# Kernel optimization log

Measured on AMD Instinct MI355X. Metric: run time of the kernel, lower is better.

The kernel has to match this reference:

```python
import jax, jax.numpy as jnp
import numpy as np

B, S_BERT, L_WORD, D = 64, 512, 256, 768
REDUC, HID, TAGS, POL = 400, 100, 5, 4


def _make_positions():
    # Each word spans 1-2 consecutive subwords; 256 words * max 2 <= 512 subwords.
    rng = np.random.default_rng(0)
    lens = rng.integers(1, 3, size=(B, L_WORD))          # [B, L] in {1,2}
    starts = np.cumsum(lens, axis=1) - lens              # exclusive prefix sum
    ends = starts + lens - 1                             # inclusive end, <= 511
    return jnp.asarray(np.stack([starts, ends], axis=-1), dtype=jnp.int32)


def setup_inputs() -> dict:
    key = jax.random.key(0)
    ks = jax.random.split(key, 8)
    s = 0.02
    return {
        "bert_vectors": jax.random.normal(ks[0], (B, S_BERT, D), jnp.float32),
        "positions": _make_positions(),
        "W_reduc": jax.random.normal(ks[1], (D, REDUC), jnp.float32) * s,
        "b_reduc": jnp.zeros((REDUC,), jnp.float32),
        "W_ap": jax.random.normal(ks[2], (REDUC, HID), jnp.float32) * s,
        "b_ap": jnp.zeros((HID,), jnp.float32),
        "W_op": jax.random.normal(ks[3], (REDUC, HID), jnp.float32) * s,
        "b_op": jnp.zeros((HID,), jnp.float32),
        "W_ap_tag": jax.random.normal(ks[4], (HID, TAGS), jnp.float32) * s,
        "b_ap_tag": jnp.zeros((TAGS,), jnp.float32),
        "W_op_tag": jax.random.normal(ks[5], (HID, TAGS), jnp.float32) * s,
        "b_op_tag": jnp.zeros((TAGS,), jnp.float32),
        # Biaffine: bias=(True, False) -> in1 gets a ones column: [HID+1, POL*HID]
        "W_bi": jax.random.normal(ks[6], (HID + 1, POL * HID), jnp.float32) * s,
    }


def _segment_mean(vectors, positions):
    # vectors: [B, S, D]; positions: [B, L, 2] inclusive (start, end) spans.
    cs = jnp.cumsum(vectors, axis=1)
    cs = jnp.concatenate([jnp.zeros_like(cs[:, :1]), cs], axis=1)   # [B, S+1, D]
    starts = positions[..., 0]
    ends = positions[..., 1]
    hi = jnp.take_along_axis(cs, (ends + 1)[..., None], axis=1)     # [B, L, D]
    lo = jnp.take_along_axis(cs, starts[..., None], axis=1)
    lens = (ends - starts + 1).astype(vectors.dtype)[..., None]
    return (hi - lo) / lens                                          # [B, L, D]


def reference(bert_vectors, positions, W_reduc, b_reduc, W_ap, b_ap, W_op, b_op,
              W_ap_tag, b_ap_tag, W_op_tag, b_op_tag, W_bi):
    pooled = _segment_mean(bert_vectors, positions)                  # [B, L, D]
    h = jax.nn.relu(pooled @ W_reduc + b_reduc)                      # [B, L, 400]
    ap = jax.nn.relu(h @ W_ap + b_ap)                                # [B, L, 100]
    op = jax.nn.relu(h @ W_op + b_op)                                # [B, L, 100]
    ap_out = ap @ W_ap_tag + b_ap_tag                                # [B, L, T]
    op_out = op @ W_op_tag + b_op_tag                                # [B, L, T]
    # Biaffine with bias=(True, False)
    ones = jnp.ones_like(ap[..., :1])
    a1 = jnp.concatenate([ap, ones], axis=-1)                        # [B, L, 101]
    affine = (a1 @ W_bi).reshape(ap.shape[0], ap.shape[1], POL, HID) # [B, L1, P, H]
    triplet = jnp.einsum('biph,bjh->bjip', affine, op)               # [B, L2, L1, P]
    return ap_out, op_out, triplet
```

## Files before the change

kernel.cpp:

```cpp
#include <hip/hip_runtime.h>
#include <hip/hip_bf16.h>

#define B_    64
#define S_    512
#define L_    256
#define D_    768
#define RED_  400
#define REDP_ 512
#define KEFF_ 416
#define HID_  100
#define HIDP_ 128
#define TAGS_ 5
#define POL_  4
#define NBI_  512
#define NAO_  256
#define BL_   (B_ * L_)

typedef __attribute__((ext_vector_type(8))) short short8;
typedef __attribute__((ext_vector_type(4))) float f32x4;
typedef __attribute__((ext_vector_type(4))) unsigned short u16x4;

#define GLOAD_LDS16(gp, lp) __builtin_amdgcn_global_load_lds( \
    (const __attribute__((address_space(1))) void*)(gp),      \
    (__attribute__((address_space(3))) void*)(lp), 16, 0, 0)

__device__ inline float bf2f(unsigned short u) {
    union { unsigned int i; float f; } c; c.i = ((unsigned)u) << 16; return c.f;
}
__device__ inline unsigned short f2bf(float f) {
    __hip_bfloat16 h = __float2bfloat16(f);
    unsigned short u;
    __builtin_memcpy(&u, &h, 2);
    return u;
}

#define SZ0 393216
#define SZ1 131072
#define SZ2 65536
#define SZ3 512
#define SZ4 256
#define PREP_TOT (SZ0 + SZ1 + SZ2 + SZ3 + SZ4)
#define PREP_BLOCKS ((PREP_TOT + 255) / 256)

__global__ __launch_bounds__(256) void prep_kernel(
    const float* __restrict__ W_reduc, const float* __restrict__ b_reduc,
    const float* __restrict__ W_ap, const float* __restrict__ b_ap,
    const float* __restrict__ W_op, const float* __restrict__ b_op,
    const float* __restrict__ W_bi,
    unsigned short* __restrict__ WtR, unsigned short* __restrict__ WtAO,
    unsigned short* __restrict__ WtBi,
    float* __restrict__ bR, float* __restrict__ bAO, float* __restrict__ bBi)
{
    int idx = blockIdx.x * 256 + threadIdx.x;
    if (idx < SZ0) {
        int n = idx / D_, k = idx - n * D_;
        float v = (n < RED_) ? W_reduc[(size_t)k * RED_ + n] : 0.f;
        WtR[idx] = f2bf(v);
    } else if (idx < SZ0 + SZ1) {
        int i = idx - SZ0;
        int n = i >> 9, k = i & 511;
        float v = 0.f;
        if (k < RED_) {
            if (n < HID_)                      v = W_ap[(size_t)k * HID_ + n];
            else if (n >= 128 && n < 128+HID_) v = W_op[(size_t)k * HID_ + (n-128)];
        }
        WtAO[i] = f2bf(v);
    } else if (idx < SZ0 + SZ1 + SZ2) {
        int i = idx - SZ0 - SZ1;
        int n = i >> 7, k = i & 127;
        int p = n >> 7, h = n & 127;
        float v = (h < HID_ && k < HID_) ? W_bi[(size_t)k * RED_ + p * HID_ + h] : 0.f;
        WtBi[i] = f2bf(v);
        if (k == 0) bBi[n] = (h < HID_) ? W_bi[(size_t)HID_ * RED_ + p * HID_ + h] : 0.f;
    } else if (idx < SZ0 + SZ1 + SZ2 + SZ3) {
        int n = idx - SZ0 - SZ1 - SZ2;
        bR[n] = (n < RED_) ? b_reduc[n] : 0.f;
    } else if (idx < PREP_TOT) {
        int n = idx - SZ0 - SZ1 - SZ2 - SZ3;
        bAO[n] = (n < 128) ? ((n < HID_) ? b_ap[n] : 0.f)
                           : (((n-128) < HID_) ? b_op[n-128] : 0.f);
    }
}

__global__ __launch_bounds__(256) void gemm1_seg_kernel(
    const float* __restrict__ bert, const int* __restrict__ pos,
    const short* __restrict__ Bt, const float* __restrict__ bias,
    unsigned short* __restrict__ Co)
{
    __shared__ __align__(16) short lds[2][10240];

    const int t  = threadIdx.x;
    const int wv = t >> 6;
    const int ln = t & 63;
    const int bm  = blockIdx.x * 64;
    const int bnh = blockIdx.y * 256;
    const int batch = bm >> 8;

    const int srow = t >> 2;
    const int skc  = (t & 3) * 8;

    const int r = bm + srow;
    const int s = pos[r * 2 + 0];
    const int e = pos[r * 2 + 1];
    const size_t rb0 = ((size_t)batch * S_ + s) * D_;
    const size_t rb1 = ((size_t)batch * S_ + e) * D_;

    f32x4 acc[4][4] = {};
    const int NT = D_ >> 5;

    {
        #pragma unroll
        for (int q = 0; q < 4; ++q) {
            const short* g = Bt + (size_t)(bnh + q * 64 + srow) * D_ + skc;
            GLOAD_LDS16(g, &lds[0][2048 + q * 2048 + wv * 512]);
        }
        f32x4 x0 = *(const f32x4*)(bert + rb0 + skc);
        f32x4 x1 = *(const f32x4*)(bert + rb0 + skc + 4);
        f32x4 y0 = *(const f32x4*)(bert + rb1 + skc);
        f32x4 y1 = *(const f32x4*)(bert + rb1 + skc + 4);
        f32x4 s0 = (x0 + y0) * 0.5f;
        f32x4 s1 = (x1 + y1) * 0.5f;
        union { short8 v; unsigned short u[8]; } o;
        #pragma unroll
        for (int j = 0; j < 4; ++j) { o.u[j] = f2bf(s0[j]); o.u[4+j] = f2bf(s1[j]); }
        *(short8*)(&lds[0][srow * 32 + skc]) = o.v;
    }
    __syncthreads();

    int cur = 0;
    const int lr = ln & 15;
    const int lk = (ln >> 4) * 8;

    for (int kt = 0; kt < NT; ++kt) {
        const bool more = (kt + 1 < NT);
        f32x4 x0, x1, y0, y1;
        if (more) {
            int col = (kt + 1) * 32 + skc;
            x0 = *(const f32x4*)(bert + rb0 + col);
            x1 = *(const f32x4*)(bert + rb0 + col + 4);
            y0 = *(const f32x4*)(bert + rb1 + col);
            y1 = *(const f32x4*)(bert + rb1 + col + 4);
            #pragma unroll
            for (int q = 0; q < 4; ++q) {
                const short* g = Bt + (size_t)(bnh + q * 64 + srow) * D_ + (kt + 1) * 32 + skc;
                GLOAD_LDS16(g, &lds[cur ^ 1][2048 + q * 2048 + wv * 512]);
            }
        }

        const short* As = &lds[cur][0];
        const short* Bs = &lds[cur][2048];
        short8 a[4], b[4];
        #pragma unroll
        for (int fi = 0; fi < 4; ++fi)
            a[fi] = *(const short8*)(As + (fi * 16 + lr) * 32 + lk);
        #pragma unroll
        for (int fj = 0; fj < 4; ++fj)
            b[fj] = *(const short8*)(Bs + (wv * 64 + fj * 16 + lr) * 32 + lk);
        #pragma unroll
        for (int fi = 0; fi < 4; ++fi)
            #pragma unroll
            for (int fj = 0; fj < 4; ++fj)
                acc[fi][fj] = __builtin_amdgcn_mfma_f32_16x16x32_bf16(
                    a[fi], b[fj], acc[fi][fj], 0, 0, 0);

        if (more) {
            f32x4 s0 = (x0 + y0) * 0.5f;
            f32x4 s1 = (x1 + y1) * 0.5f;
            union { short8 v; unsigned short u[8]; } o;
            #pragma unroll
            for (int j = 0; j < 4; ++j) { o.u[j] = f2bf(s0[j]); o.u[4+j] = f2bf(s1[j]); }
            *(short8*)(&lds[cur ^ 1][srow * 32 + skc]) = o.v;
        }

        __syncthreads();
        cur ^= 1;
    }

    const int row0 = bm + (ln >> 4) * 4;
    const int col0 = bnh + wv * 64 + lr;
    #pragma unroll
    for (int fi = 0; fi < 4; ++fi)
        #pragma unroll
        for (int rr = 0; rr < 4; ++rr) {
            int row = row0 + fi * 16 + rr;
            #pragma unroll
            for (int fj = 0; fj < 4; ++fj) {
                int col = col0 + fj * 16;
                float v = fmaxf(acc[fi][fj][rr] + bias[col], 0.f);
                Co[(size_t)row * REDP_ + col] = f2bf(v);
            }
        }
}

__global__ __launch_bounds__(256) void gemm23_tag_kernel(
    const short* __restrict__ A, const short* __restrict__ Bt,
    const float* __restrict__ bias,
    unsigned short* __restrict__ apOut, unsigned short* __restrict__ opOut,
    const float* __restrict__ Wap_tag, const float* __restrict__ bap_tag,
    const float* __restrict__ Wop_tag, const float* __restrict__ bop_tag,
    float* __restrict__ out_tag)
{
    __shared__ __align__(16) short lds[2][8192];
    __shared__ float tagf[128 * 101];
    __shared__ float Wtag[HID_ * TAGS_];
    __shared__ float Btag[TAGS_];

    const int t  = threadIdx.x;
    const int wv = t >> 6;
    const int ln = t & 63;
    const int wm = wv >> 1;
    const int wn = wv & 1;
    const int bm = blockIdx.x * 128;
    const int bn = blockIdx.y * 128;
    const int half = blockIdx.y;

    const float* Wt = half ? Wop_tag : Wap_tag;
    const float* bt = half ? bop_tag : bap_tag;
    for (int i = t; i < HID_ * TAGS_; i += 256) Wtag[i] = Wt[i];
    if (t < TAGS_) Btag[t] = bt[t];

    const int srow = t >> 2;
    const int skc  = (t & 3) * 8;
    const int NT = KEFF_ >> 5;

    f32x4 acc[4][4] = {};

    {
        #pragma unroll
        for (int q = 0; q < 2; ++q) {
            const short* g = A + (size_t)(bm + q * 64 + srow) * REDP_ + skc;
            GLOAD_LDS16(g, &lds[0][q * 2048 + wv * 512]);
        }
        #pragma unroll
        for (int q = 0; q < 2; ++q) {
            const short* g = Bt + (size_t)(bn + q * 64 + srow) * REDP_ + skc;
            GLOAD_LDS16(g, &lds[0][4096 + q * 2048 + wv * 512]);
        }
    }
    __syncthreads();

    int cur = 0;
    const int lr = ln & 15;
    const int lk = (ln >> 4) * 8;

    for (int kt = 0; kt < NT; ++kt) {
        if (kt + 1 < NT) {
            int k0 = (kt + 1) << 5;
            #pragma unroll
            for (int q = 0; q < 2; ++q) {
                const short* g = A + (size_t)(bm + q * 64 + srow) * REDP_ + k0 + skc;
                GLOAD_LDS16(g, &lds[cur ^ 1][q * 2048 + wv * 512]);
            }
            #pragma unroll
            for (int q = 0; q < 2; ++q) {
                const short* g = Bt + (size_t)(bn + q * 64 + srow) * REDP_ + k0 + skc;
                GLOAD_LDS16(g, &lds[cur ^ 1][4096 + q * 2048 + wv * 512]);
            }
        }

        const short* As = &lds[cur][0];
        const short* Bs = &lds[cur][4096];
        short8 a[4], b[4];
        #pragma unroll
        for (int fi = 0; fi < 4; ++fi)
            a[fi] = *(const short8*)(As + (wm * 64 + fi * 16 + lr) * 32 + lk);
        #pragma unroll
        for (int fj = 0; fj < 4; ++fj)
            b[fj] = *(const short8*)(Bs + (wn * 64 + fj * 16 + lr) * 32 + lk);
        #pragma unroll
        for (int fi = 0; fi < 4; ++fi)
            #pragma unroll
            for (int fj = 0; fj < 4; ++fj)
                acc[fi][fj] = __builtin_amdgcn_mfma_f32_16x16x32_bf16(
                    a[fi], b[fj], acc[fi][fj], 0, 0, 0);

        __syncthreads();
        cur ^= 1;
    }

    unsigned short* Co = half ? opOut : apOut;
    const int rl0 = wm * 64 + (ln >> 4) * 4;
    const int cl0 = wn * 64 + lr;
    #pragma unroll
    for (int fi = 0; fi < 4; ++fi)
        #pragma unroll
        for (int r = 0; r < 4; ++r) {
            int rl = rl0 + fi * 16 + r;
            #pragma unroll
            for (int fj = 0; fj < 4; ++fj) {
                int cl = cl0 + fj * 16;
                float v = fmaxf(acc[fi][fj][r] + bias[bn + cl], 0.f);
                Co[(size_t)(bm + rl) * 128 + cl] = f2bf(v);
                if (cl < 101) tagf[rl * 101 + cl] = v;
            }
        }
    __syncthreads();

    if (t < 128) {
        float s[TAGS_];
        #pragma unroll
        for (int g = 0; g < TAGS_; ++g) s[g] = Btag[g];
        const float* rowp = &tagf[t * 101];
        for (int k = 0; k < HID_; ++k) {
            float x = rowp[k];
            #pragma unroll
            for (int g = 0; g < TAGS_; ++g) s[g] += x * Wtag[k * TAGS_ + g];
        }
        float* o = out_tag + (size_t)half * (BL_ * TAGS_) + (size_t)(bm + t) * TAGS_;
        #pragma unroll
        for (int g = 0; g < TAGS_; ++g) o[g] = s[g];
    }
}

__global__ __launch_bounds__(256) void affine_kernel(
    const short* __restrict__ ap, const short* __restrict__ WtBi,
    const float* __restrict__ bBi, unsigned short* __restrict__ affine)
{
    __shared__ __align__(16) short As[16384];
    __shared__ __align__(16) short Bs[16384];

    const int t  = threadIdx.x;
    const int wv = t >> 6;
    const int ln = t & 63;
    const int wm = wv >> 1;
    const int wn = wv & 1;
    const int bm = blockIdx.x * 128;
    const int bn = blockIdx.y * 128;

    const int rsub = ln >> 2;
    const int j8   = (ln & 3) * 8;

    #pragma unroll
    for (int i = 0; i < 8; ++i) {
        int ks = i >> 1, hf = i & 1;
        int rloc = wv * 32 + hf * 16;
        const short* gA = ap + (size_t)(bm + rloc + rsub) * HIDP_ + ks * 32 + j8;
        GLOAD_LDS16(gA, &As[ks * 4096 + rloc * 32]);
        const short* gB = WtBi + (size_t)(bn + rloc + rsub) * HIDP_ + ks * 32 + j8;
        GLOAD_LDS16(gB, &Bs[ks * 4096 + rloc * 32]);
    }
    __syncthreads();

    const int lr = ln & 15;
    const int lk = (ln >> 4) * 8;
    f32x4 acc[4][4] = {};

    #pragma unroll
    for (int ks = 0; ks < 4; ++ks) {
        short8 a[4], b[4];
        #pragma unroll
        for (int fi = 0; fi < 4; ++fi)
            a[fi] = *(const short8*)(As + ks * 4096 + (wm * 64 + fi * 16 + lr) * 32 + lk);
        #pragma unroll
        for (int fj = 0; fj < 4; ++fj)
            b[fj] = *(const short8*)(Bs + ks * 4096 + (wn * 64 + fj * 16 + lr) * 32 + lk);
        #pragma unroll
        for (int fi = 0; fi < 4; ++fi)
            #pragma unroll
            for (int fj = 0; fj < 4; ++fj)
                acc[fi][fj] = __builtin_amdgcn_mfma_f32_16x16x32_bf16(
                    a[fi], b[fj], acc[fi][fj], 0, 0, 0);
    }

    const int row0 = bm + wm * 64 + (ln >> 4) * 4;
    const int col0 = bn + wn * 64 + lr;
    #pragma unroll
    for (int fi = 0; fi < 4; ++fi)
        #pragma unroll
        for (int r = 0; r < 4; ++r) {
            int row = row0 + fi * 16 + r;
            #pragma unroll
            for (int fj = 0; fj < 4; ++fj) {
                int col = col0 + fj * 16;
                affine[(size_t)row * NBI_ + col] = f2bf(acc[fi][fj][r] + bBi[col]);
            }
        }
}

__global__ __launch_bounds__(256) void triplet_kernel(
    const short* __restrict__ op, const short* __restrict__ affine,
    float* __restrict__ out)
{
    __shared__ __align__(16) short As[16384];
    __shared__ __align__(16) short Bs[16384];

    const int t  = threadIdx.x;
    const int wv = t >> 6;
    const int ln = t & 63;
    const int wm = wv >> 1;
    const int wn = wv & 1;
    const int bm = blockIdx.x * 128;
    const int bn = blockIdx.y * 128;
    const int b  = blockIdx.z;

    const short* Ab = op     + (size_t)b * 256 * HIDP_;
    const short* Bb = affine + (size_t)b * 256 * NBI_;

    const int rsub = ln >> 2;
    const int j8   = (ln & 3) * 8;

    #pragma unroll
    for (int i = 0; i < 8; ++i) {
        int ks = i >> 1, hf = i & 1;
        int rloc = wv * 32 + hf * 16;
        const short* gA = Ab + (size_t)(bm + rloc + rsub) * HIDP_ + ks * 32 + j8;
        GLOAD_LDS16(gA, &As[ks * 4096 + rloc * 32]);
        int ip = bn + rloc + rsub;
        const short* gB = Bb + (size_t)(ip >> 2) * NBI_ + (ip & 3) * HIDP_ + ks * 32 + j8;
        GLOAD_LDS16(gB, &Bs[ks * 4096 + rloc * 32]);
    }
    __syncthreads();

    const int lr = ln & 15;
    const int lk = (ln >> 4) * 8;
    f32x4 acc[4][4] = {};

    #pragma unroll
    for (int ks = 0; ks < 4; ++ks) {
        short8 a[4], bf[4];
        #pragma unroll
        for (int fi = 0; fi < 4; ++fi)
            a[fi] = *(const short8*)(As + ks * 4096 + (wm * 64 + fi * 16 + lr) * 32 + lk);
        #pragma unroll
        for (int fj = 0; fj < 4; ++fj)
            bf[fj] = *(const short8*)(Bs + ks * 4096 + (wn * 64 + fj * 16 + lr) * 32 + lk);
        #pragma unroll
        for (int fi = 0; fi < 4; ++fi)
            #pragma unroll
            for (int fj = 0; fj < 4; ++fj)
                acc[fi][fj] = __builtin_amdgcn_mfma_f32_16x16x32_bf16(
                    a[fi], bf[fj], acc[fi][fj], 0, 0, 0);
    }

    float* O = out + (size_t)b * 256 * 1024;
    const int row0 = bm + wm * 64 + (ln >> 4) * 4;
    const int col0 = bn + wn * 64 + lr;
    #pragma unroll
    for (int fi = 0; fi < 4; ++fi)
        #pragma unroll
        for (int r = 0; r < 4; ++r) {
            int row = row0 + fi * 16 + r;
            #pragma unroll
            for (int fj = 0; fj < 4; ++fj)
                O[(size_t)row * 1024 + col0 + fj * 16] = acc[fi][fj][r];
        }
}

extern "C" void kernel_launch(void* const* d_in, const int* in_sizes, int n_in,
                              void* d_out, int out_size, void* d_ws, size_t ws_size,
                              hipStream_t stream)
{
    const float* bert     = (const float*)d_in[0];
    const int*   pos      = (const int*)  d_in[1];
    const float* W_reduc  = (const float*)d_in[2];
    const float* b_reduc  = (const float*)d_in[3];
    const float* W_ap     = (const float*)d_in[4];
    const float* b_ap     = (const float*)d_in[5];
    const float* W_op     = (const float*)d_in[6];
    const float* b_op     = (const float*)d_in[7];
    const float* W_ap_tag = (const float*)d_in[8];
    const float* b_ap_tag = (const float*)d_in[9];
    const float* W_op_tag = (const float*)d_in[10];
    const float* b_op_tag = (const float*)d_in[11];
    const float* W_bi     = (const float*)d_in[12];

    float* out = (float*)d_out;

    char* ws = (char*)d_ws;
    unsigned short* h      = (unsigned short*)ws; ws += (size_t)BL_ * REDP_ * 2;
    unsigned short* ap     = (unsigned short*)ws; ws += (size_t)BL_ * HIDP_ * 2;
    unsigned short* opv    = (unsigned short*)ws; ws += (size_t)BL_ * HIDP_ * 2;
    unsigned short* affine = (unsigned short*)ws; ws += (size_t)BL_ * NBI_ * 2;
    unsigned short* WtR    = (unsigned short*)ws; ws += (size_t)REDP_ * D_ * 2;
    unsigned short* WtAO   = (unsigned short*)ws; ws += (size_t)NAO_ * REDP_ * 2;
    unsigned short* WtBi   = (unsigned short*)ws; ws += (size_t)NBI_ * HIDP_ * 2;
    float* bR  = (float*)ws;  ws += REDP_ * 4;
    float* bAO = (float*)ws;  ws += NAO_ * 4;
    float* bBi = (float*)ws;  ws += NBI_ * 4;

    prep_kernel<<<PREP_BLOCKS, 256, 0, stream>>>(
        W_reduc, b_reduc, W_ap, b_ap, W_op, b_op, W_bi,
        WtR, WtAO, WtBi, bR, bAO, bBi);

    gemm1_seg_kernel<<<dim3(BL_ / 64, 2), 256, 0, stream>>>(
        bert, pos, (const short*)WtR, bR, h);

    gemm23_tag_kernel<<<dim3(BL_ / 128, 2), 256, 0, stream>>>(
        (const short*)h, (const short*)WtAO, bAO, ap, opv,
        W_ap_tag, b_ap_tag, W_op_tag, b_op_tag, out);

    affine_kernel<<<dim3(BL_ / 128, NBI_ / 128), 256, 0, stream>>>(
        (const short*)ap, (const short*)WtBi, bBi, affine);

    triplet_kernel<<<dim3(2, 8, B_), 256, 0, stream>>>(
        (const short*)opv, (const short*)affine, out + 2 * BL_ * TAGS_);
}
```

Before: 80.09 us.

## Fuse biaffine projection into triplet GEMM, keeping affine tile in LDS

Merges the affine and triplet kernels into one. Each block computes a 32-row slab of ap @ W_bi directly into shared memory in the layout the triplet GEMM expects, then loops over both 128-row halves of op. This removes the bf16 affine intermediate's global write and read and one kernel launch. In exchange the biaffine GEMM reads W_bi fragments straight from global memory with small MFMA tiles. The grid also shrinks to 512 blocks, each doing two triplet tiles serially with extra barriers.

Result: faster. 77.14 us (median of 2 runs) (-3.7%).

```diff
diff --git a/kernel.cpp b/kernel.cpp
--- a/kernel.cpp
+++ b/kernel.cpp
@@ -312,20 +312,25 @@
     }
 }
 
-__global__ __launch_bounds__(256) void affine_kernel(
-    const short* __restrict__ ap, const short* __restrict__ WtBi,
-    const float* __restrict__ bBi, unsigned short* __restrict__ affine)
+__global__ __launch_bounds__(256) void bi_triplet_kernel(
+    const short* __restrict__ op, const short* __restrict__ ap,
+    const short* __restrict__ WtBi, const float* __restrict__ bBi,
+    float* __restrict__ out)
 {
     __shared__ __align__(16) short As[16384];
     __shared__ __align__(16) short Bs[16384];
+    __shared__ __align__(16) short Aap[4096];
 
     const int t  = threadIdx.x;
     const int wv = t >> 6;
     const int ln = t & 63;
     const int wm = wv >> 1;
     const int wn = wv & 1;
-    const int bm = blockIdx.x * 128;
-    const int bn = blockIdx.y * 128;
+    const int ipt = blockIdx.x;
+    const int b   = blockIdx.y;
+
+    const short* opB = op + (size_t)b * 256 * HIDP_;
+    const short* apB = ap + ((size_t)b * 256 + ipt * 32) * HIDP_;
 
     const int rsub = ln >> 2;
     const int j8   = (ln & 3) * 8;
@@ -334,116 +339,104 @@
     for (int i = 0; i < 8; ++i) {
         int ks = i >> 1, hf = i & 1;
         int rloc = wv * 32 + hf * 16;
-        const short* gA = ap + (size_t)(bm + rloc + rsub) * HIDP_ + ks * 32 + j8;
+        const short* gA = opB + (size_t)(rloc + rsub) * HIDP_ + ks * 32 + j8;
         GLOAD_LDS16(gA, &As[ks * 4096 + rloc * 32]);
-        const short* gB = WtBi + (size_t)(bn + rloc + rsub) * HIDP_ + ks * 32 + j8;
-        GLOAD_LDS16(gB, &Bs[ks * 4096 + rloc * 32]);
+    }
+    #pragma unroll
+    for (int q = 0; q < 2; ++q) {
+        int kf   = q * 2 + (wv >> 1);
+        int irow = (wv & 1) * 16 + (ln >> 2);
+        const short* gA = apB + (size_t)irow * HIDP_ + kf * 32 + (ln & 3) * 8;
+        GLOAD_LDS16(gA, &Aap[q * 2048 + wv * 512]);
     }
     __syncthreads();
 
     const int lr = ln & 15;
     const int lk = (ln >> 4) * 8;
-    f32x4 acc[4][4] = {};
-
-    #pragma unroll
-    for (int ks = 0; ks < 4; ++ks) {
-        short8 a[4], b[4];
+    const int hbase = wv * 32;
+
+    #pragma unroll
+    for (int p = 0; p < 4; ++p) {
+        f32x4 acc2[2][2] = {};
+        const short* Wp = WtBi + (size_t)(p * 128) * HIDP_;
+        #pragma unroll
+        for (int kf = 0; kf < 4; ++kf) {
+            short8 a2[2], b2[2];
+            #pragma unroll
+            for (int fm = 0; fm < 2; ++fm)
+                a2[fm] = *(const short8*)(Aap + kf * 1024 + (fm * 16 + lr) * 32 + lk);
+            #pragma unroll
+            for (int fn = 0; fn < 2; ++fn)
+                b2[fn] = *(const short8*)(Wp + (size_t)(hbase + fn * 16 + lr) * HIDP_ + kf * 32 + lk);
+            #pragma unroll
+            for (int fm = 0; fm < 2; ++fm)
+                #pragma unroll
+                for (int fn = 0; fn < 2; ++fn)
+                    acc2[fm][fn] = __builtin_amdgcn_mfma_f32_16x16x32_bf16(
+                        a2[fm], b2[fn], acc2[fm][fn], 0, 0, 0);
+        }
+        #pragma unroll
+        for (int fm = 0; fm < 2; ++fm)
+            #pragma unroll
+            for (int fn = 0; fn < 2; ++fn) {
+                int h = hbase + fn * 16 + lr;
+                float bias = bBi[p * 128 + h];
+                #pragma unroll
+                for (int r = 0; r < 4; ++r) {
+                    int i = fm * 16 + (ln >> 4) * 4 + r;
+                    float v = acc2[fm][fn][r] + bias;
+                    Bs[(h >> 5) * 4096 + (i * 4 + p) * 32 + (h & 31)] = (short)f2bf(v);
+                }
+            }
+    }
+    __syncthreads();
+
+    float* Ob = out + (size_t)b * 256 * 1024;
+    #pragma unroll
+    for (int jt = 0; jt < 2; ++jt) {
+        f32x4 acc[4][4] = {};
+        #pragma unroll
+        for (int ks = 0; ks < 4; ++ks) {
+            short8 a[4], bf[4];
+            #pragma unroll
+            for (int fi = 0; fi < 4; ++fi)
+                a[fi] = *(const short8*)(As + ks * 4096 + (wm * 64 + fi * 16 + lr) * 32 + lk);
+            #pragma unroll
+            for (int fj = 0; fj < 4; ++fj)
+                bf[fj] = *(const short8*)(Bs + ks * 4096 + (wn * 64 + fj * 16 + lr) * 32 + lk);
+            #pragma unroll
+            for (int fi = 0; fi < 4; ++fi)
+                #pragma unroll
+                for (int fj = 0; fj < 4; ++fj)
+                    acc[fi][fj] = __builtin_amdgcn_mfma_f32_16x16x32_bf16(
+                        a[fi], bf[fj], acc[fi][fj], 0, 0, 0);
+        }
+
+        if (jt == 0) {
+            __syncthreads();
+            #pragma unroll
+            for (int i = 0; i < 8; ++i) {
+                int ks = i >> 1, hf = i & 1;
+                int rloc = wv * 32 + hf * 16;
+                const short* gA = opB + (size_t)(128 + rloc + rsub) * HIDP_ + ks * 32 + j8;
+                GLOAD_LDS16(gA, &As[ks * 4096 + rloc * 32]);
+            }
+        }
+
+        const int row0 = jt * 128 + wm * 64 + (ln >> 4) * 4;
+        const int col0 = ipt * 128 + wn * 64 + lr;
         #pragma unroll
         for (int fi = 0; fi < 4; ++fi)
-            a[fi] = *(const short8*)(As + ks * 4096 + (wm * 64 + fi * 16 + lr) * 32 + lk);
-        #pragma unroll
-        for (int fj = 0; fj < 4; ++fj)
-            b[fj] = *(const short8*)(Bs + ks * 4096 + (wn * 64 + fj * 16 + lr) * 32 + lk);
-        #pragma unroll
-        for (int fi = 0; fi < 4; ++fi)
-            #pragma unroll
-            for (int fj = 0; fj < 4; ++fj)
-                acc[fi][fj] = __builtin_amdgcn_mfma_f32_16x16x32_bf16(
-                    a[fi], b[fj], acc[fi][fj], 0, 0, 0);
-    }
-
-    const int row0 = bm + wm * 64 + (ln >> 4) * 4;
-    const int col0 = bn + wn * 64 + lr;
-    #pragma unroll
-    for (int fi = 0; fi < 4; ++fi)
-        #pragma unroll
-        for (int r = 0; r < 4; ++r) {
-            int row = row0 + fi * 16 + r;
-            #pragma unroll
-            for (int fj = 0; fj < 4; ++fj) {
-                int col = col0 + fj * 16;
-                affine[(size_t)row * NBI_ + col] = f2bf(acc[fi][fj][r] + bBi[col]);
-            }
-        }
-}
-
-__global__ __launch_bounds__(256) void triplet_kernel(
-    const short* __restrict__ op, const short* __restrict__ affine,
-    float* __restrict__ out)
-{
-    __shared__ __align__(16) short As[16384];
-    __shared__ __align__(16) short Bs[16384];
-
-    const int t  = threadIdx.x;
-    const int wv = t >> 6;
-    const int ln = t & 63;
-    const int wm = wv >> 1;
-    const int wn = wv & 1;
-    const int bm = blockIdx.x * 128;
-    const int bn = blockIdx.y * 128;
-    const int b  = blockIdx.z;
-
-    const short* Ab = op     + (size_t)b * 256 * HIDP_;
-    const short* Bb = affine + (size_t)b * 256 * NBI_;
-
-    const int rsub = ln >> 2;
-    const int j8   = (ln & 3) * 8;
-
-    #pragma unroll
-    for (int i = 0; i < 8; ++i) {
-        int ks = i >> 1, hf = i & 1;
-        int rloc = wv * 32 + hf * 16;
-        const short* gA = Ab + (size_t)(bm + rloc + rsub) * HIDP_ + ks * 32 + j8;
-        GLOAD_LDS16(gA, &As[ks * 4096 + rloc * 32]);
-        int ip = bn + rloc + rsub;
-        const short* gB = Bb + (size_t)(ip >> 2) * NBI_ + (ip & 3) * HIDP_ + ks * 32 + j8;
-        GLOAD_LDS16(gB, &Bs[ks * 4096 + rloc * 32]);
-    }
-    __syncthreads();
-
-    const int lr = ln & 15;
-    const int lk = (ln >> 4) * 8;
-    f32x4 acc[4][4] = {};
-
-    #pragma unroll
-    for (int ks = 0; ks < 4; ++ks) {
-        short8 a[4], bf[4];
-        #pragma unroll
-        for (int fi = 0; fi < 4; ++fi)
-            a[fi] = *(const short8*)(As + ks * 4096 + (wm * 64 + fi * 16 + lr) * 32 + lk);
-        #pragma unroll
-        for (int fj = 0; fj < 4; ++fj)
-            bf[fj] = *(const short8*)(Bs + ks * 4096 + (wn * 64 + fj * 16 + lr) * 32 + lk);
-        #pragma unroll
-        for (int fi = 0; fi < 4; ++fi)
-            #pragma unroll
-            for (int fj = 0; fj < 4; ++fj)
-                acc[fi][fj] = __builtin_amdgcn_mfma_f32_16x16x32_bf16(
-                    a[fi], bf[fj], acc[fi][fj], 0, 0, 0);
-    }
-
-    float* O = out + (size_t)b * 256 * 1024;
-    const int row0 = bm + wm * 64 + (ln >> 4) * 4;
-    const int col0 = bn + wn * 64 + lr;
-    #pragma unroll
-    for (int fi = 0; fi < 4; ++fi)
-        #pragma unroll
-        for (int r = 0; r < 4; ++r) {
-            int row = row0 + fi * 16 + r;
-            #pragma unroll
-            for (int fj = 0; fj < 4; ++fj)
-                O[(size_t)row * 1024 + col0 + fj * 16] = acc[fi][fj][r];
-        }
+            #pragma unroll
+            for (int r = 0; r < 4; ++r) {
+                int row = row0 + fi * 16 + r;
+                #pragma unroll
+                for (int fj = 0; fj < 4; ++fj)
+                    Ob[(size_t)row * 1024 + col0 + fj * 16] = acc[fi][fj][r];
+            }
+
+        if (jt == 0) __syncthreads();
+    }
 }
 
 extern "C" void kernel_launch(void* const* d_in, const int* in_sizes, int n_in,
@@ -470,7 +463,6 @@
     unsigned short* h      = (unsigned short*)ws; ws += (size_t)BL_ * REDP_ * 2;
     unsigned short* ap     = (unsigned short*)ws; ws += (size_t)BL_ * HIDP_ * 2;
     unsigned short* opv    = (unsigned short*)ws; ws += (size_t)BL_ * HIDP_ * 2;
-    unsigned short* affine = (unsigned short*)ws; ws += (size_t)BL_ * NBI_ * 2;
     unsigned short* WtR    = (unsigned short*)ws; ws += (size_t)REDP_ * D_ * 2;
     unsigned short* WtAO   = (unsigned short*)ws; ws += (size_t)NAO_ * REDP_ * 2;
     unsigned short* WtBi   = (unsigned short*)ws; ws += (size_t)NBI_ * HIDP_ * 2;
@@ -489,9 +481,7 @@
         (const short*)h, (const short*)WtAO, bAO, ap, opv,
         W_ap_tag, b_ap_tag, W_op_tag, b_op_tag, out);
 
-    affine_kernel<<<dim3(BL_ / 128, NBI_ / 128), 256, 0, stream>>>(
-        (const short*)ap, (const short*)WtBi, bBi, affine);
-
-    triplet_kernel<<<dim3(2, 8, B_), 256, 0, stream>>>(
-        (const short*)opv, (const short*)affine, out + 2 * BL_ * TAGS_);
-}
+    bi_triplet_kernel<<<dim3(8, B_), 256, 0, stream>>>(
+        (const short*)opv, (const short*)ap, (const short*)WtBi, bBi,
+        out + 2 * BL_ * TAGS_);
+}
```
